# Kernel tuning notes

Hardware: AMD Instinct MI355X
Metric: run time of the kernel (lower is better)

## Reference

```python
import jax, jax.numpy as jnp
import numpy as np

NUM_ATOMS = 100000
NUM_BONDS = 200000
MAX_NB = 6
ATOM_FDIM = 133
BOND_FDIM = 147
HIDDEN = 300
DEPTH = 4
NUM_MOLS = 8192


def setup_inputs() -> dict:
    key = jax.random.key(0)
    ks = jax.random.split(key, 10)
    f_atoms = jax.random.normal(ks[0], (NUM_ATOMS, ATOM_FDIM), dtype=jnp.float32)
    f_bonds = jax.random.normal(ks[1], (NUM_BONDS, BOND_FDIM), dtype=jnp.float32)
    a2b = jax.random.randint(ks[2], (NUM_ATOMS, MAX_NB), 0, NUM_BONDS, dtype=jnp.int32)
    b2a = jax.random.randint(ks[3], (NUM_BONDS,), 0, NUM_ATOMS, dtype=jnp.int32)
    b2revb = jax.random.randint(ks[4], (NUM_BONDS,), 0, NUM_BONDS, dtype=jnp.int32)
    mol_ids = jnp.sort(jax.random.randint(ks[5], (NUM_ATOMS,), 0, NUM_MOLS, dtype=jnp.int32))
    s = 1.0 / np.sqrt(HIDDEN)
    W_i = jax.random.uniform(ks[6], (BOND_FDIM, HIDDEN), jnp.float32, -s, s)
    W_h = jax.random.uniform(ks[7], (HIDDEN, HIDDEN), jnp.float32, -s, s)
    W_o = jax.random.uniform(ks[8], (ATOM_FDIM + HIDDEN, HIDDEN), jnp.float32, -s, s)
    b_o = jax.random.uniform(ks[9], (HIDDEN,), jnp.float32, -s, s)
    return {"f_atoms": f_atoms, "f_bonds": f_bonds, "W_i": W_i, "W_h": W_h,
            "W_o": W_o, "b_o": b_o, "a2b": a2b, "b2a": b2a, "b2revb": b2revb,
            "mol_ids": mol_ids}


def reference(f_atoms, f_bonds, W_i, W_h, W_o, b_o, a2b, b2a, b2revb, mol_ids):
    # initial bond messages: W_i then activation (bias=False)
    inp = f_bonds @ W_i                       # [B, H]
    message = jax.nn.relu(inp)
    for _ in range(DEPTH - 1):
        nei = message[a2b]                    # [A, MAX_NB, H] gather
        a_message = nei.sum(axis=1)           # [A, H]
        rev_message = message[b2revb]         # [B, H]
        message = a_message[b2a] - rev_message
        message = jax.nn.relu(inp + message @ W_h)
    # final atom readout
    a_message = message[a2b].sum(axis=1)      # [A, H]
    a_input = jnp.concatenate([f_atoms, a_message], axis=1)
    atom_hiddens = jax.nn.relu(a_input @ W_o + b_o)
    # per-molecule mean aggregation (== chemprop a_scope loop with 'mean')
    sums = jax.ops.segment_sum(atom_hiddens, mol_ids, num_segments=NUM_MOLS)
    counts = jax.ops.segment_sum(jnp.ones((NUM_ATOMS,), jnp.float32), mol_ids,
                                 num_segments=NUM_MOLS)
    return sums / jnp.maximum(counts, 1.0)[:, None]
```

## Files before the change

### kernel.cpp

```cpp
#include <hip/hip_runtime.h>


#define DEVFN static __device__ __forceinline__

typedef __attribute__((ext_vector_type(8))) __bf16 bf16x8;
typedef __attribute__((ext_vector_type(4))) float floatx4;

DEVFN unsigned short f2bf(float f) {
    unsigned int u = __float_as_uint(f);
    u += 0x7FFFu + ((u >> 16) & 1u);
    return (unsigned short)(u >> 16);
}
DEVFN float bf2f(unsigned int u) { return __uint_as_float(u << 16); }

DEVFN unsigned int bfsub2(unsigned int a, unsigned int m) {
    float lo = bf2f(a & 0xffffu) - bf2f(m & 0xffffu);
    float hi = bf2f(a >> 16) - bf2f(m >> 16);
    return (unsigned int)f2bf(lo) | ((unsigned int)f2bf(hi) << 16);
}
DEVFN uint4 bfsub8(uint4 a, uint4 m) {
    return make_uint4(bfsub2(a.x, m.x), bfsub2(a.y, m.y),
                      bfsub2(a.z, m.z), bfsub2(a.w, m.w));
}

__global__ __launch_bounds__(256) void dbg_fill(float* out, int n, float v) {
    int t = blockIdx.x * 256 + threadIdx.x;
    if (t < n) out[t] = v;
}

__global__ __launch_bounds__(256) void prep_wih(const float* __restrict__ Wi,
                                                const float* __restrict__ Wh,
                                                unsigned short* __restrict__ Wt) {
    int t = blockIdx.x * 256 + threadIdx.x;
    if (t >= 320 * 480) return;
    int j = t & 7;
    int lane = (t >> 3) & 63;
    int rest = t >> 9;
    int kt = rest % 15, nb = rest / 15;
    int n = nb * 16 + (lane & 15);
    int k = kt * 32 + (lane >> 4) * 8 + j;
    float v = 0.f;
    if (n < 300) {
        if (k < 147) v = Wi[k * 300 + n];
        else if (k >= 160 && k < 460) v = Wh[(k - 160) * 300 + n];
    }
    Wt[t] = f2bf(v);
}

__global__ __launch_bounds__(256) void prep_wto(const float* __restrict__ Wo,
                                                unsigned short* __restrict__ Wt) {
    int t = blockIdx.x * 256 + threadIdx.x;
    if (t >= 320 * 448) return;
    int j = t & 7;
    int lane = (t >> 3) & 63;
    int rest = t >> 9;
    int kt = rest % 14, nb = rest / 14;
    int n = nb * 16 + (lane & 15);
    int k = kt * 32 + (lane >> 4) * 8 + j;
    float v = 0.f;
    if (n < 300) {
        if (k < 300) v = Wo[(133 + k) * 300 + n];
        else if (k >= 304 && k < 437) v = Wo[(k - 304) * 300 + n];
    }
    Wt[t] = f2bf(v);
}

__global__ __launch_bounds__(256) void pad_bonds(const float* __restrict__ fb,
                                                 unsigned short* __restrict__ out) {
    int t = blockIdx.x * 256 + threadIdx.x;
    if (t >= 200000 * 20) return;
    int b = t / 20, c = t - b * 20;
    unsigned int o[4];
#pragma unroll
    for (int p = 0; p < 4; ++p) {
        int sc = c * 8 + p * 2;
        float v0 = (sc < 147) ? fb[(size_t)b * 147 + sc] : 0.f;
        float v1 = (sc + 1 < 147) ? fb[(size_t)b * 147 + sc + 1] : 0.f;
        o[p] = (unsigned int)f2bf(v0) | ((unsigned int)f2bf(v1) << 16);
    }
    *(uint4*)(out + (size_t)b * 160 + c * 8) = make_uint4(o[0], o[1], o[2], o[3]);
}

__global__ __launch_bounds__(256) void atoms_concat(const float* __restrict__ fa,
                                                    unsigned short* __restrict__ concat) {
    int t = blockIdx.x * 256 + threadIdx.x;
    if (t >= 100000 * 18) return;
    int a = t / 18, c = t - a * 18;
    unsigned int o[4];
#pragma unroll
    for (int p = 0; p < 4; ++p) {
        int sc = c * 8 + p * 2;
        float v0 = (sc < 133) ? fa[(size_t)a * 133 + sc] : 0.f;
        float v1 = (sc + 1 < 133) ? fa[(size_t)a * 133 + sc + 1] : 0.f;
        o[p] = (unsigned int)f2bf(v0) | ((unsigned int)f2bf(v1) << 16);
    }
    *(uint4*)(concat + (size_t)a * 448 + 304 + c * 8) = make_uint4(o[0], o[1], o[2], o[3]);
}

template <int CH>
__global__ __launch_bounds__(256) void gather_sum(const unsigned short* __restrict__ msg,
                                                  const int* __restrict__ a2b,
                                                  unsigned short* __restrict__ out,
                                                  int ostride, int nA) {
    int t = blockIdx.x * 256 + threadIdx.x;
    if (t >= nA * CH) return;
    int a = t / CH, c = t - a * CH;
    float s[8] = {0, 0, 0, 0, 0, 0, 0, 0};
#pragma unroll
    for (int j = 0; j < 6; ++j) {
        int b = a2b[a * 6 + j];
        uint4 v = *(const uint4*)(msg + (size_t)b * 320 + c * 8);
        s[0] += bf2f(v.x & 0xffffu); s[1] += bf2f(v.x >> 16);
        s[2] += bf2f(v.y & 0xffffu); s[3] += bf2f(v.y >> 16);
        s[4] += bf2f(v.z & 0xffffu); s[5] += bf2f(v.z >> 16);
        s[6] += bf2f(v.w & 0xffffu); s[7] += bf2f(v.w >> 16);
    }
    unsigned int o[4];
#pragma unroll
    for (int p = 0; p < 4; ++p)
        o[p] = (unsigned int)f2bf(s[2 * p]) | ((unsigned int)f2bf(s[2 * p + 1]) << 16);
    *(uint4*)(out + (size_t)a * ostride + c * 8) = make_uint4(o[0], o[1], o[2], o[3]);
}

template <int KT0, int KT1, int MODE, int WNB>
__global__ __launch_bounds__(256) void gemm_k(const unsigned short* __restrict__ A0,
                                              int a0s,
                                              const unsigned short* __restrict__ amsg,
                                              const unsigned short* __restrict__ msg,
                                              const int* __restrict__ b2a,
                                              const int* __restrict__ b2revb,
                                              const unsigned short* __restrict__ Wf,
                                              unsigned short* __restrict__ outp,
                                              float* __restrict__ hid,
                                              const float* __restrict__ bo, int M) {
    constexpr int KT = KT0 + KT1;
    __shared__ unsigned short As[2 * 5120];

    const int tid = threadIdx.x;
    const int lane = tid & 63;
    const int wave = tid >> 6;
    const int wm = wave & 1, wn = wave >> 1;
    const int l16 = lane & 15, quad = lane >> 4;

    int m0, n0;
    {
        const int bid = blockIdx.x;
        const int MB = (int)(gridDim.x >> 1);
        const int mfull = (MB >> 3) << 3;
        const int FULL = mfull << 1;
        int mb, nh;
        if (bid < FULL) {
            nh = (bid >> 3) & 1;
            mb = ((bid >> 4) << 3) + (bid & 7);
        } else {
            const int r = bid - FULL;
            const int rem = MB - mfull;
            nh = (r >= rem) ? 1 : 0;
            mb = mfull + r - nh * rem;
        }
        m0 = mb * 128;
        n0 = nh * 160;
    }

    const int arow = tid >> 1, ahalf = tid & 1;
    const int gr = min(m0 + arow, M - 1);
    const unsigned short* a0p = A0 + (size_t)gr * a0s + ahalf * 16;
    const unsigned short* a1p = nullptr;
    const unsigned short* m1p = nullptr;
    if (KT1 > 0) {
        a1p = amsg + (size_t)b2a[gr] * 320 + ahalf * 16;
        m1p = msg + (size_t)b2revb[gr] * 320 + ahalf * 16;
    }

    const int nbase = (n0 >> 4) + wn * 5;
    const unsigned short* pB[5];
#pragma unroll
    for (int tn = 0; tn < 5; ++tn)
        pB[tn] = Wf + (size_t)(nbase + tn) * (WNB * 512) + lane * 8;

    int aoff[4];
#pragma unroll
    for (int tm = 0; tm < 4; ++tm)
        aoff[tm] = (wm * 64 + tm * 16 + l16) * 40 + quad * 8;

    floatx4 acc[4][5];
#pragma unroll
    for (int tm = 0; tm < 4; ++tm)
#pragma unroll
        for (int tn = 0; tn < 5; ++tn) acc[tm][tn] = (floatx4){0.f, 0.f, 0.f, 0.f};

    struct Set { uint4 va0, va1, vm0, vm1, b0, b1, b2, b3, b4; };
    Set P, Q;

    auto ldg = [&](int kt, Set& s) {
        if (kt < KT0) {
            s.va0 = *(const uint4*)(a0p + kt * 32);
            s.va1 = *(const uint4*)(a0p + kt * 32 + 8);
        } else {
            int ko = (kt - KT0) * 32;
            s.va0 = *(const uint4*)(a1p + ko);
            s.va1 = *(const uint4*)(a1p + ko + 8);
            s.vm0 = *(const uint4*)(m1p + ko);
            s.vm1 = *(const uint4*)(m1p + ko + 8);
        }
        s.b0 = *(const uint4*)(pB[0] + kt * 512);
        s.b1 = *(const uint4*)(pB[1] + kt * 512);
        s.b2 = *(const uint4*)(pB[2] + kt * 512);
        s.b3 = *(const uint4*)(pB[3] + kt * 512);
        s.b4 = *(const uint4*)(pB[4] + kt * 512);
    };
    auto stw = [&](int buf, int kt, const Set& s) {
        unsigned short* ab = As + buf * 5120 + arow * 40 + ahalf * 16;
        if (kt < KT0) {
            *(uint4*)(ab) = s.va0;
            *(uint4*)(ab + 8) = s.va1;
        } else {
            *(uint4*)(ab) = bfsub8(s.va0, s.vm0);
            *(uint4*)(ab + 8) = bfsub8(s.va1, s.vm1);
        }
    };
    auto barsync = [&]() {
        asm volatile("s_waitcnt lgkmcnt(0)" ::: "memory");
        __builtin_amdgcn_sched_barrier(0);
        __builtin_amdgcn_s_barrier();
        __builtin_amdgcn_sched_barrier(0);
    };
    auto compute = [&](int buf, const Set& s) {
        bf16x8 av[4];
#pragma unroll
        for (int tm = 0; tm < 4; ++tm)
            av[tm] = *(const bf16x8*)(As + buf * 5120 + aoff[tm]);
        const bf16x8 bv[5] = {
            __builtin_bit_cast(bf16x8, s.b0), __builtin_bit_cast(bf16x8, s.b1),
            __builtin_bit_cast(bf16x8, s.b2), __builtin_bit_cast(bf16x8, s.b3),
            __builtin_bit_cast(bf16x8, s.b4)};
#pragma unroll
        for (int tn = 0; tn < 5; ++tn)
#pragma unroll
            for (int tm = 0; tm < 4; ++tm)
                acc[tm][tn] = __builtin_amdgcn_mfma_f32_16x16x32_bf16(av[tm], bv[tn], acc[tm][tn], 0, 0, 0);
    };

    ldg(0, P);
    if (KT > 1) ldg(1, Q);
    stw(0, 0, P);
    barsync();

#pragma unroll
    for (int kt = 0; kt < KT; ++kt) {
        const int buf = kt & 1;
        if ((kt & 1) == 0) {
            compute(buf, P);
            if (kt + 2 < KT) ldg(kt + 2, P);
            if (kt + 1 < KT) { stw(buf ^ 1, kt + 1, Q); barsync(); }
        } else {
            compute(buf, Q);
            if (kt + 2 < KT) ldg(kt + 2, Q);
            if (kt + 1 < KT) { stw(buf ^ 1, kt + 1, P); barsync(); }
        }
    }

    float bias[5];
    if (MODE == 2) {
#pragma unroll
        for (int tn = 0; tn < 5; ++tn) {
            int col = n0 + wn * 80 + tn * 16 + l16;
            bias[tn] = (col < 300) ? bo[col] : 0.f;
        }
    }
#pragma unroll
    for (int tm = 0; tm < 4; ++tm) {
        const int r0 = m0 + wm * 64 + tm * 16 + quad * 4;
#pragma unroll
        for (int tn = 0; tn < 5; ++tn) {
            const int col = n0 + wn * 80 + tn * 16 + l16;
#pragma unroll
            for (int i = 0; i < 4; ++i) {
                int r = r0 + i;
                if (r >= M) continue;
                float c = acc[tm][tn][i];
                if (MODE == 2) {
                    if (col < 300) hid[(size_t)r * 300 + col] = fmaxf(c + bias[tn], 0.f);
                } else {
                    outp[(size_t)r * 320 + col] = f2bf(fmaxf(c, 0.f));
                }
            }
        }
    }
}

__global__ __launch_bounds__(320) void mean_k(const float* __restrict__ hid,
                                              const int* __restrict__ mol_ids,
                                              float* __restrict__ out, int nA) {
    int mol = blockIdx.x;
    int lo, hi;
    {
        int l = 0, h = nA;
        while (l < h) { int m = (l + h) >> 1; if (mol_ids[m] < mol) l = m + 1; else h = m; }
        lo = l;
    }
    {
        int l = lo, h = nA;
        while (l < h) { int m = (l + h) >> 1; if (mol_ids[m] < mol + 1) l = m + 1; else h = m; }
        hi = l;
    }
    int col = threadIdx.x;
    if (col >= 300) return;
    float s = 0.f;
    for (int a = lo; a < hi; ++a) s += hid[(size_t)a * 300 + col];
    int cnt = hi - lo;
    out[(size_t)mol * 300 + col] = s / (float)(cnt > 0 ? cnt : 1);
}

extern "C" void kernel_launch(void* const* d_in, const int* in_sizes, int n_in,
                              void* d_out, int out_size, void* d_ws, size_t ws_size,
                              hipStream_t stream) {
    (void)in_sizes; (void)n_in;
    const float* f_atoms = (const float*)d_in[0];
    const float* f_bonds = (const float*)d_in[1];
    const float* W_i     = (const float*)d_in[2];
    const float* W_h     = (const float*)d_in[3];
    const float* W_o     = (const float*)d_in[4];
    const float* b_o     = (const float*)d_in[5];
    const int*   a2b     = (const int*)d_in[6];
    const int*   b2a     = (const int*)d_in[7];
    const int*   b2revb  = (const int*)d_in[8];
    const int*   mol_ids = (const int*)d_in[9];

    const size_t sz_wih  = 320ull * 480 * 2;
    const size_t sz_wto  = 320ull * 448 * 2;
    const size_t sz_fbp  = 200000ull * 160 * 2;
    const size_t sz_amsg = 100000ull * 320 * 2;
    const size_t sz_msg  = 200000ull * 320 * 2;
    const size_t need = sz_wih + sz_wto + sz_fbp + sz_amsg + 2 * sz_msg;

    if (ws_size < need) {
        dbg_fill<<<(out_size + 255) / 256, 256, 0, stream>>>(
            (float*)d_out, out_size, (float)(ws_size >> 20));
        return;
    }

    char* ws = (char*)d_ws;
    unsigned short* wih  = (unsigned short*)(ws);
    unsigned short* wto  = (unsigned short*)(ws + sz_wih);
    unsigned short* fbp  = (unsigned short*)(ws + sz_wih + sz_wto);
    unsigned short* amsg = (unsigned short*)(ws + sz_wih + sz_wto + sz_fbp);
    unsigned short* msgA = (unsigned short*)(ws + sz_wih + sz_wto + sz_fbp + sz_amsg);
    unsigned short* msgB = (unsigned short*)(ws + sz_wih + sz_wto + sz_fbp + sz_amsg + sz_msg);
    unsigned short* concat = msgA;
    float*          hid    = (float*)msgB;

    prep_wih<<<600, 256, 0, stream>>>(W_i, W_h, wih);
    prep_wto<<<560, 256, 0, stream>>>(W_o, wto);
    pad_bonds<<<15625, 256, 0, stream>>>(f_bonds, fbp);

    gemm_k<5, 0, 0, 15><<<dim3(3126), 256, 0, stream>>>(
        fbp, 160, nullptr, nullptr, nullptr, nullptr, wih, msgA, nullptr, nullptr, 200000);

    unsigned short* cur = msgA;
    unsigned short* other = msgB;
    for (int d = 0; d < 3; ++d) {
        gather_sum<40><<<15625, 256, 0, stream>>>(cur, a2b, amsg, 320, 100000);
        gemm_k<5, 10, 0, 15><<<dim3(3126), 256, 0, stream>>>(
            fbp, 160, amsg, cur, b2a, b2revb, wih, other, nullptr, nullptr, 200000);
        unsigned short* t = cur; cur = other; other = t;
    }

    gather_sum<38><<<14844, 256, 0, stream>>>(cur, a2b, concat, 448, 100000);
    atoms_concat<<<7032, 256, 0, stream>>>(f_atoms, concat);
    gemm_k<14, 0, 2, 14><<<dim3(1564), 256, 0, stream>>>(
        concat, 448, nullptr, nullptr, nullptr, nullptr, wto, nullptr, hid, b_o, 100000);
    mean_k<<<8192, 320, 0, stream>>>(hid, mol_ids, (float*)d_out, 100000);
}
```

Baseline: 1.273 ms.

## Give each wave a private LDS A-tile to drop block barriers in GEMM

```diff
diff --git a/kernel.cpp b/kernel.cpp
--- a/kernel.cpp
+++ b/kernel.cpp
@@ -134,7 +134,7 @@
                                               float* __restrict__ hid,
                                               const float* __restrict__ bo, int M) {
     constexpr int KT = KT0 + KT1;
-    __shared__ unsigned short As[2 * 5120];
+    __shared__ unsigned short As[4 * 2 * 2560];
 
     const int tid = threadIdx.x;
     const int lane = tid & 63;
@@ -162,15 +162,15 @@
         n0 = nh * 160;
     }
 
-    const int arow = tid >> 1, ahalf = tid & 1;
-    const int gr = min(m0 + arow, M - 1);
-    const unsigned short* a0p = A0 + (size_t)gr * a0s + ahalf * 16;
+    const int ar = min(m0 + wm * 64 + lane, M - 1);
+    const unsigned short* a0p = A0 + (size_t)ar * a0s;
     const unsigned short* a1p = nullptr;
     const unsigned short* m1p = nullptr;
     if (KT1 > 0) {
-        a1p = amsg + (size_t)b2a[gr] * 320 + ahalf * 16;
-        m1p = msg + (size_t)b2revb[gr] * 320 + ahalf * 16;
-    }
+        a1p = amsg + (size_t)b2a[ar] * 320;
+        m1p = msg + (size_t)b2revb[ar] * 320;
+    }
+    unsigned short* myAs = As + wave * 5120;
 
     const int nbase = (n0 >> 4) + wn * 5;
     const unsigned short* pB[5];
@@ -181,7 +181,7 @@
     int aoff[4];
 #pragma unroll
     for (int tm = 0; tm < 4; ++tm)
-        aoff[tm] = (wm * 64 + tm * 16 + l16) * 40 + quad * 8;
+        aoff[tm] = (tm * 16 + l16) * 40 + ((quad ^ (l16 & 3)) * 8);
 
     floatx4 acc[4][5];
 #pragma unroll
@@ -189,62 +189,49 @@
 #pragma unroll
         for (int tn = 0; tn < 5; ++tn) acc[tm][tn] = (floatx4){0.f, 0.f, 0.f, 0.f};
 
-    struct Set { uint4 va0, va1, vm0, vm1, b0, b1, b2, b3, b4; };
+    struct Set { uint4 a[4]; uint4 b[5]; };
     Set P, Q;
 
     auto ldg = [&](int kt, Set& s) {
         if (kt < KT0) {
-            s.va0 = *(const uint4*)(a0p + kt * 32);
-            s.va1 = *(const uint4*)(a0p + kt * 32 + 8);
+#pragma unroll
+            for (int c = 0; c < 4; ++c)
+                s.a[c] = *(const uint4*)(a0p + kt * 32 + c * 8);
         } else {
-            int ko = (kt - KT0) * 32;
-            s.va0 = *(const uint4*)(a1p + ko);
-            s.va1 = *(const uint4*)(a1p + ko + 8);
-            s.vm0 = *(const uint4*)(m1p + ko);
-            s.vm1 = *(const uint4*)(m1p + ko + 8);
-        }
-        s.b0 = *(const uint4*)(pB[0] + kt * 512);
-        s.b1 = *(const uint4*)(pB[1] + kt * 512);
-        s.b2 = *(const uint4*)(pB[2] + kt * 512);
-        s.b3 = *(const uint4*)(pB[3] + kt * 512);
-        s.b4 = *(const uint4*)(pB[4] + kt * 512);
+            const int ko = (kt - KT0) * 32;
+#pragma unroll
+            for (int c = 0; c < 4; ++c) {
+                uint4 va = *(const uint4*)(a1p + ko + c * 8);
+                uint4 vm = *(const uint4*)(m1p + ko + c * 8);
+                s.a[c] = bfsub8(va, vm);
+            }
+        }
+#pragma unroll
+        for (int tn = 0; tn < 5; ++tn)
+            s.b[tn] = *(const uint4*)(pB[tn] + kt * 512);
     };
-    auto stw = [&](int buf, int kt, const Set& s) {
-        unsigned short* ab = As + buf * 5120 + arow * 40 + ahalf * 16;
-        if (kt < KT0) {
-            *(uint4*)(ab) = s.va0;
-            *(uint4*)(ab + 8) = s.va1;
-        } else {
-            *(uint4*)(ab) = bfsub8(s.va0, s.vm0);
-            *(uint4*)(ab + 8) = bfsub8(s.va1, s.vm1);
-        }
-    };
-    auto barsync = [&]() {
-        asm volatile("s_waitcnt lgkmcnt(0)" ::: "memory");
-        __builtin_amdgcn_sched_barrier(0);
-        __builtin_amdgcn_s_barrier();
-        __builtin_amdgcn_sched_barrier(0);
+    auto stw = [&](int buf, const Set& s) {
+        unsigned short* ab = myAs + buf * 2560 + lane * 40;
+#pragma unroll
+        for (int c = 0; c < 4; ++c)
+            *(uint4*)(ab + ((c ^ (lane & 3)) * 8)) = s.a[c];
     };
     auto compute = [&](int buf, const Set& s) {
         bf16x8 av[4];
 #pragma unroll
         for (int tm = 0; tm < 4; ++tm)
-            av[tm] = *(const bf16x8*)(As + buf * 5120 + aoff[tm]);
-        const bf16x8 bv[5] = {
-            __builtin_bit_cast(bf16x8, s.b0), __builtin_bit_cast(bf16x8, s.b1),
-            __builtin_bit_cast(bf16x8, s.b2), __builtin_bit_cast(bf16x8, s.b3),
-            __builtin_bit_cast(bf16x8, s.b4)};
+            av[tm] = *(const bf16x8*)(myAs + buf * 2560 + aoff[tm]);
 #pragma unroll
         for (int tn = 0; tn < 5; ++tn)
 #pragma unroll
             for (int tm = 0; tm < 4; ++tm)
-                acc[tm][tn] = __builtin_amdgcn_mfma_f32_16x16x32_bf16(av[tm], bv[tn], acc[tm][tn], 0, 0, 0);
+                acc[tm][tn] = __builtin_amdgcn_mfma_f32_16x16x32_bf16(
+                    av[tm], __builtin_bit_cast(bf16x8, s.b[tn]), acc[tm][tn], 0, 0, 0);
     };
 
     ldg(0, P);
     if (KT > 1) ldg(1, Q);
-    stw(0, 0, P);
-    barsync();
+    stw(0, P);
 
 #pragma unroll
     for (int kt = 0; kt < KT; ++kt) {
@@ -252,11 +239,11 @@
         if ((kt & 1) == 0) {
             compute(buf, P);
             if (kt + 2 < KT) ldg(kt + 2, P);
-            if (kt + 1 < KT) { stw(buf ^ 1, kt + 1, Q); barsync(); }
+            if (kt + 1 < KT) stw(buf ^ 1, Q);
         } else {
             compute(buf, Q);
             if (kt + 2 < KT) ldg(kt + 2, Q);
-            if (kt + 1 < KT) { stw(buf ^ 1, kt + 1, P); barsync(); }
+            if (kt + 1 < KT) stw(buf ^ 1, P);
         }
     }
 
```

Measured after the change: 1.489 ms. 1.17x slower.
